# Kernel optimization log

Measured on AMD Instinct MI355X. Metric: run time of the kernel, lower is better.

## Reference

```python
import math
import jax, jax.numpy as jnp
import numpy as np

D_MODEL = 1024
NHEAD = 16
DK = D_MODEL // NHEAD
FACTOR = 5
B, L = 4, 8192
U = max(1, min(FACTOR * math.ceil(math.log(L + 1)), L))  # 50


def setup_inputs() -> dict:
    key = jax.random.key(0)
    ks = jax.random.split(key, 10)
    s = 1.0 / math.sqrt(D_MODEL)
    inp = {
        "x": jax.random.normal(ks[0], (B, L, D_MODEL), dtype=jnp.float32),
        "Wq": jax.random.normal(ks[1], (D_MODEL, D_MODEL), dtype=jnp.float32) * s,
        "bq": jnp.zeros((D_MODEL,), dtype=jnp.float32),
        "Wk": jax.random.normal(ks[2], (D_MODEL, D_MODEL), dtype=jnp.float32) * s,
        "bk": jnp.zeros((D_MODEL,), dtype=jnp.float32),
        "Wv": jax.random.normal(ks[3], (D_MODEL, D_MODEL), dtype=jnp.float32) * s,
        "bv": jnp.zeros((D_MODEL,), dtype=jnp.float32),
        "Wo": jax.random.normal(ks[4], (D_MODEL, D_MODEL), dtype=jnp.float32) * s,
        "bo": jnp.zeros((D_MODEL,), dtype=jnp.float32),
        # randperm(L)[:U] sample of key positions (constant, like torch.randperm)
        "idx_k": jax.random.permutation(ks[5], L)[:U].astype(jnp.int32),
    }
    return inp


def reference(x, Wq, bq, Wk, bk, Wv, bv, Wo, bo, idx_k):
    Bv, Lv, _ = x.shape
    H, dk = NHEAD, DK
    u = idx_k.shape[0]
    scale = 1.0 / math.sqrt(dk)

    # projections -> [B, H, L, dk]
    Q = (x @ Wq.T + bq).reshape(Bv, Lv, H, dk).transpose(0, 2, 1, 3)
    K = (x @ Wk.T + bk).reshape(Bv, Lv, H, dk).transpose(0, 2, 1, 3)
    V = (x @ Wv.T + bv).reshape(Bv, Lv, H, dk).transpose(0, 2, 1, 3)

    # sampled scores against u random keys: [B, H, L, u]
    K_samp = K[:, :, idx_k, :]
    scores = jnp.einsum("bhld,bhud->bhlu", Q, K_samp) * scale
    M = scores.max(-1) - scores.mean(-1)                 # [B, H, L]
    _, top_idx = jax.lax.top_k(M, u)                      # [B, H, u]

    # gather selected queries and attend against ALL keys
    Q_top = jnp.take_along_axis(Q, top_idx[..., None], axis=2)   # [B, H, u, dk]
    attn = jax.nn.softmax(jnp.einsum("bhud,bhld->bhul", Q_top, K) * scale, axis=-1)
    ctx_top = jnp.einsum("bhul,bhld->bhud", attn, V)              # [B, H, u, dk]

    # mean(V) fallback, scatter selected contexts back
    ctx = jnp.broadcast_to(V.mean(axis=2, keepdims=True), (Bv, H, Lv, dk))
    bidx = jnp.arange(Bv)[:, None, None]
    hidx = jnp.arange(H)[None, :, None]
    ctx = ctx.at[bidx, hidx, top_idx].set(ctx_top)

    ctx = ctx.transpose(0, 2, 1, 3).reshape(Bv, Lv, H * dk)
    return ctx @ Wo.T + bo
```

## Files before the change

kernel.cpp:

```cpp
#include <hip/hip_runtime.h>
#include <hip/hip_bf16.h>

#define B_ 4
#define L_ 8192
#define D_ 1024
#define H_ 16
#define SCALE 0.125f
#define NC 8
#define QPAD 64
#define RS 72

typedef __attribute__((ext_vector_type(8))) short bf16x8;
typedef __attribute__((ext_vector_type(4))) float f32x4;

__device__ __forceinline__ void gl2lds16(const void* g, void* s) {
    __builtin_amdgcn_global_load_lds(
        (const __attribute__((address_space(1))) unsigned int*)g,
        (__attribute__((address_space(3))) unsigned int*)s, 16, 0, 0);
}

__device__ __forceinline__ unsigned short bfbits(float a) {
    __hip_bfloat16 h = __float2bfloat16(a);
    return *(unsigned short*)&h;
}
__device__ __forceinline__ float bf2f(unsigned short u) {
    return __uint_as_float(((unsigned)u) << 16);
}

__global__ __launch_bounds__(256) void split3_kernel(const float* __restrict__ in,
        unsigned short* __restrict__ ph, unsigned short* __restrict__ pm,
        unsigned short* __restrict__ pl, int n4) {
    int i = blockIdx.x * 256 + threadIdx.x;
    if (i >= n4) return;
    float4 v = ((const float4*)in)[i];
    float c[4] = {v.x, v.y, v.z, v.w};
    unsigned short h[4], m[4], l[4];
    #pragma unroll
    for (int j = 0; j < 4; ++j) {
        float a = c[j];
        unsigned short hb = bfbits(a);
        float rh = a - bf2f(hb);
        unsigned short mb = bfbits(rh);
        float rm = rh - bf2f(mb);
        h[j] = hb; m[j] = mb; l[j] = bfbits(rm);
    }
    ((ushort4*)ph)[i] = *(ushort4*)h;
    ((ushort4*)pm)[i] = *(ushort4*)m;
    ((ushort4*)pl)[i] = *(ushort4*)l;
}

__global__ __launch_bounds__(256) void split2_kernel(const float* __restrict__ in,
        unsigned short* __restrict__ ph, unsigned short* __restrict__ pm, int n4) {
    int i = blockIdx.x * 256 + threadIdx.x;
    if (i >= n4) return;
    float4 v = ((const float4*)in)[i];
    float c[4] = {v.x, v.y, v.z, v.w};
    unsigned short h[4], m[4];
    #pragma unroll
    for (int j = 0; j < 4; ++j) {
        float a = c[j];
        unsigned short hb = bfbits(a);
        float rh = a - bf2f(hb);
        h[j] = hb; m[j] = bfbits(rh);
    }
    ((ushort4*)ph)[i] = *(ushort4*)h;
    ((ushort4*)pm)[i] = *(ushort4*)m;
}

__global__ __launch_bounds__(256) void xmean_kernel(const float* __restrict__ x,
                                                    float* __restrict__ xmean) {
    int c = blockIdx.x;
    int j = blockIdx.y * 256 + threadIdx.x;
    int b = blockIdx.z;
    const float* xp = x + ((size_t)b * L_ + (size_t)c * 256) * D_ + j;
    float s = 0.f;
    for (int l = 0; l < 256; ++l) s += xp[(size_t)l * D_];
    atomicAdd(&xmean[b * D_ + j], s * (1.0f / L_));
}

__global__ __launch_bounds__(256) void vecmat_kernel(const float* __restrict__ in,
                                                     const float* __restrict__ W,
                                                     const float* __restrict__ bias,
                                                     float* __restrict__ out) {
    __shared__ float vs[D_];
    int b = blockIdx.y;
    int j = blockIdx.x * 256 + threadIdx.x;
    for (int t = threadIdx.x; t < D_; t += 256) vs[t] = in[b * D_ + t];
    __syncthreads();
    const float* wr = W + (size_t)j * D_;
    float acc = 0.f;
    #pragma unroll 4
    for (int k = 0; k < D_; k += 4) {
        float4 w4 = *(const float4*)(wr + k);
        acc += vs[k] * w4.x + vs[k + 1] * w4.y + vs[k + 2] * w4.z + vs[k + 3] * w4.w;
    }
    out[b * D_ + j] = acc + bias[j];
}

__global__ __launch_bounds__(256) void ksamp_kernel(const float* __restrict__ x,
                                                    const float* __restrict__ Wk,
                                                    const float* __restrict__ bk,
                                                    const int* __restrict__ idx_k,
                                                    float* __restrict__ Ksamp, int U) {
    __shared__ float vs[D_];
    int u = blockIdx.x, b = blockIdx.y;
    int row = idx_k[u];
    const float* xp = x + ((size_t)b * L_ + row) * D_;
    for (int t = threadIdx.x; t < D_; t += 256) vs[t] = xp[t];
    __syncthreads();
    #pragma unroll
    for (int r = 0; r < 4; ++r) {
        int j = r * 256 + threadIdx.x;
        const float* wr = Wk + (size_t)j * D_;
        float acc = 0.f;
        #pragma unroll 4
        for (int k = 0; k < D_; k += 4) {
            float4 w4 = *(const float4*)(wr + k);
            acc += vs[k] * w4.x + vs[k + 1] * w4.y + vs[k + 2] * w4.z + vs[k + 3] * w4.w;
        }
        Ksamp[((size_t)b * U + u) * D_ + j] = acc + bk[j];
    }
}

#define TM 128
#define TN 128
#define BK 32
#define TSZ (TM * BK)

__global__ __launch_bounds__(256) void qkv_mfma(
    const unsigned short* __restrict__ xh, const unsigned short* __restrict__ xm,
    const unsigned short* __restrict__ xl,
    const unsigned short* __restrict__ qh, const unsigned short* __restrict__ qm,
    const unsigned short* __restrict__ ql,
    const unsigned short* __restrict__ kh, const unsigned short* __restrict__ km,
    const unsigned short* __restrict__ vh, const unsigned short* __restrict__ vm,
    const float* __restrict__ bq, const float* __restrict__ bk2, const float* __restrict__ bv,
    float* __restrict__ Q, __hip_bfloat16* __restrict__ Kb, __hip_bfloat16* __restrict__ Vb) {
    __shared__ __align__(16) unsigned short As[3][TSZ];
    __shared__ __align__(16) unsigned short Bs[3][TSZ];

    const int n0 = blockIdx.x * TN;
    const int m0 = blockIdx.y * TM;
    const int tid = threadIdx.x;

    const float* bias; int which; int nb;
    if (n0 < 1024)      { which = 0; nb = n0;        bias = bq;  }
    else if (n0 < 2048) { which = 1; nb = n0 - 1024; bias = bk2; }
    else                { which = 2; nb = n0 - 2048; bias = bv;  }

    const int srow = tid >> 2;
    const int scol = (tid & 3) * 8;

    const int wave = tid >> 6;
    const int lane = tid & 63;
    const int wm = (wave & 1) * 64;
    const int wn = (wave >> 1) * 64;
    const int fr = lane & 15;
    const int fk = (lane >> 4) * 8;
    const int rbase = (lane >> 4) * 4;

    f32x4 acc[4][4];
    #pragma unroll
    for (int i = 0; i < 4; ++i)
        #pragma unroll
        for (int j = 0; j < 4; ++j)
            acc[i][j] = (f32x4){0.f, 0.f, 0.f, 0.f};

    const size_t aBase = (size_t)(m0 + srow) * D_ + scol;
    const size_t bBase = (size_t)(nb + srow) * D_ + scol;

    bf16x8 af[4], bfv[4];
    auto loadA = [&](const unsigned short* t) {
        #pragma unroll
        for (int i = 0; i < 4; ++i)
            af[i] = *(const bf16x8*)(t + (wm + i * 16 + fr) * BK + fk);
    };
    auto loadB = [&](const unsigned short* t) {
        #pragma unroll
        for (int j = 0; j < 4; ++j)
            bfv[j] = *(const bf16x8*)(t + (wn + j * 16 + fr) * BK + fk);
    };
    auto prod = [&]() {
        #pragma unroll
        for (int i = 0; i < 4; ++i)
            #pragma unroll
            for (int j = 0; j < 4; ++j)
                acc[i][j] = __builtin_amdgcn_mfma_f32_16x16x32_bf16(
                    af[i], bfv[j], acc[i][j], 0, 0, 0);
    };
    auto stage = [&](const unsigned short* g, unsigned short* s, int kt, size_t base) {
        gl2lds16(g + base + kt, s + tid * 8);
        gl2lds16(g + base + (size_t)64 * D_ + kt, s + tid * 8 + 2048);
    };

    if (which == 0) {
        for (int kt = 0; kt < D_; kt += BK) {
            stage(xh, &As[0][0], kt, aBase);
            stage(xm, &As[1][0], kt, aBase);
            stage(xl, &As[2][0], kt, aBase);
            stage(qh, &Bs[0][0], kt, bBase);
            stage(qm, &Bs[1][0], kt, bBase);
            stage(ql, &Bs[2][0], kt, bBase);
            __syncthreads();
            loadA(&As[0][0]); loadB(&Bs[0][0]); prod();
            loadB(&Bs[1][0]); prod();
            loadB(&Bs[2][0]); prod();
            loadA(&As[1][0]); loadB(&Bs[0][0]); prod();
            loadB(&Bs[1][0]); prod();
            loadA(&As[2][0]); loadB(&Bs[0][0]); prod();
            __syncthreads();
        }
    } else {
        const unsigned short* Bh = (which == 1) ? kh : vh;
        const unsigned short* Bm = (which == 1) ? km : vm;
        for (int kt = 0; kt < D_; kt += BK) {
            stage(xh, &As[0][0], kt, aBase);
            stage(xm, &As[1][0], kt, aBase);
            stage(Bh, &Bs[0][0], kt, bBase);
            stage(Bm, &Bs[1][0], kt, bBase);
            __syncthreads();
            loadA(&As[0][0]); loadB(&Bs[0][0]); prod();
            loadB(&Bs[1][0]); prod();
            loadA(&As[1][0]); loadB(&Bs[0][0]); prod();
            __syncthreads();
        }
    }

    float biasv[4];
    #pragma unroll
    for (int j = 0; j < 4; ++j) biasv[j] = bias[nb + wn + j * 16 + fr];

    #pragma unroll
    for (int i = 0; i < 4; ++i) {
        #pragma unroll
        for (int r = 0; r < 4; ++r) {
            size_t row = (size_t)(m0 + wm + i * 16 + rbase + r);
            #pragma unroll
            for (int j = 0; j < 4; ++j) {
                float v = acc[i][j][r] + biasv[j];
                int n = nb + wn + j * 16 + fr;
                if (which == 0)      Q[row * D_ + n] = v;
                else if (which == 1) Kb[row * D_ + n] = __float2bfloat16(v);
                else                 Vb[row * D_ + n] = __float2bfloat16(v);
            }
        }
    }
}

__global__ __launch_bounds__(256) void m_kernel(const float* __restrict__ Q,
                                                const float* __restrict__ Ksamp,
                                                float* __restrict__ M, int U) {
    __shared__ float ks[64 * 64];
    int lc = blockIdx.x, h = blockIdx.y, b = blockIdx.z;
    for (int t = threadIdx.x; t < U * 64; t += 256) {
        int u = t >> 6, d = t & 63;
        ks[t] = Ksamp[((size_t)b * U + u) * D_ + h * 64 + d];
    }
    __syncthreads();
    int l = lc * 256 + threadIdx.x;
    const float* qp = Q + ((size_t)b * L_ + l) * D_ + h * 64;
    float q[64];
    #pragma unroll
    for (int i = 0; i < 16; ++i) *(float4*)&q[i * 4] = *(const float4*)(qp + i * 4);
    float mx = -INFINITY, sm = 0.f;
    for (int u = 0; u < U; ++u) {
        const float* kp = &ks[u * 64];
        float dot = 0.f;
        #pragma unroll
        for (int d = 0; d < 64; ++d) dot = fmaf(q[d], kp[d], dot);
        dot *= SCALE;
        mx = fmaxf(mx, dot);
        sm += dot;
    }
    M[((size_t)(b * H_ + h)) * L_ + l] = mx - sm / (float)U;
}

__global__ __launch_bounds__(256) void topk_kernel(const float* __restrict__ M,
                                                   int* __restrict__ topidx, int U) {
    __shared__ float vals[L_];
    __shared__ float wv[4];
    __shared__ int   wi[4];
    __shared__ int   sbest;
    int bh = blockIdx.x;
    const float* mp = M + (size_t)bh * L_;
    for (int t = threadIdx.x; t < L_; t += 256) vals[t] = mp[t];
    __syncthreads();

    float bv = -INFINITY; int bi = 0x7fffffff;
    for (int t = threadIdx.x; t < L_; t += 256) {
        float v = vals[t];
        if (v > bv || (v == bv && t < bi)) { bv = v; bi = t; }
    }
    const int lane = threadIdx.x & 63, wave = threadIdx.x >> 6;

    for (int u = 0; u < U; ++u) {
        float rv = bv; int ri = bi;
        #pragma unroll
        for (int s = 1; s < 64; s <<= 1) {
            float v2 = __shfl_xor(rv, s, 64);
            int   i2 = __shfl_xor(ri, s, 64);
            if (v2 > rv || (v2 == rv && i2 < ri)) { rv = v2; ri = i2; }
        }
        if (lane == 0) { wv[wave] = rv; wi[wave] = ri; }
        __syncthreads();
        if (threadIdx.x == 0) {
            float fv = wv[0]; int fi = wi[0];
            #pragma unroll
            for (int w = 1; w < 4; ++w) {
                if (wv[w] > fv || (wv[w] == fv && wi[w] < fi)) { fv = wv[w]; fi = wi[w]; }
            }
            topidx[bh * U + u] = fi;
            sbest = fi;
            vals[fi] = -INFINITY;
        }
        __syncthreads();
        int fi = sbest;
        if ((fi & 255) == threadIdx.x) {
            bv = -INFINITY; bi = 0x7fffffff;
            for (int t = threadIdx.x; t < L_; t += 256) {
                float v = vals[t];
                if (v > bv || (v == bv && t < bi)) { bv = v; bi = t; }
            }
        }
    }
}

__global__ __launch_bounds__(256) void attn_mfma(const float* __restrict__ Q,
        const __hip_bfloat16* __restrict__ Kb, const __hip_bfloat16* __restrict__ Vb,
        const int* __restrict__ topidx,
        float* __restrict__ part_m, float* __restrict__ part_s,
        float* __restrict__ part_acc, int U) {
    __shared__ __align__(16) unsigned short Qh[QPAD * RS];
    __shared__ __align__(16) unsigned short Qm[QPAD * RS];
    __shared__ __align__(16) unsigned short Ks[64 * RS];
    __shared__ __align__(16) unsigned short Vt[64 * RS];
    __shared__ __align__(16) unsigned short Ph[QPAD * RS];

    const int c = blockIdx.x, h = blockIdx.y, b = blockIdx.z;
    const int bh = b * H_ + h;
    const int tid = threadIdx.x;
    const int wave = tid >> 6, lane = tid & 63;
    const int w16 = wave * 16;
    const int fr = lane & 15;
    const int quad = lane >> 4;
    const int fk = quad * 8;
    const int l0 = c * (L_ / NC);

    {
        int u = tid >> 2;
        int d0 = (tid & 3) * 16;
        unsigned short hbuf[16], mbuf[16];
        if (u < U) {
            int row = topidx[bh * U + u];
            const float* qp = Q + ((size_t)b * L_ + row) * D_ + h * 64 + d0;
            #pragma unroll
            for (int i = 0; i < 16; ++i) {
                float v = qp[i] * SCALE;
                unsigned short hb = bfbits(v);
                hbuf[i] = hb;
                mbuf[i] = bfbits(v - bf2f(hb));
            }
        } else {
            #pragma unroll
            for (int i = 0; i < 16; ++i) { hbuf[i] = 0; mbuf[i] = 0; }
        }
        #pragma unroll
        for (int i = 0; i < 2; ++i) {
            *(uint4*)&Qh[u * RS + d0 + i * 8] = ((uint4*)hbuf)[i];
            *(uint4*)&Qm[u * RS + d0 + i * 8] = ((uint4*)mbuf)[i];
        }
    }

    const int kkey = tid >> 3, kd0 = (tid & 7) * 8;
    const int vkey = tid >> 2, vd0 = (tid & 3) * 16;
    const __hip_bfloat16* kbase = Kb + ((size_t)b * L_ + l0) * D_ + h * 64;
    const __hip_bfloat16* vbase = Vb + ((size_t)b * L_ + l0) * D_ + h * 64;

    uint4 kr0, kr1, vr0, vr1;
    auto loadKV = [&](int t) {
        const __hip_bfloat16* kp = kbase + (size_t)t * 64 * D_;
        const __hip_bfloat16* vp = vbase + (size_t)t * 64 * D_ + (size_t)vkey * D_ + vd0;
        kr0 = *(const uint4*)(kp + (size_t)kkey * D_ + kd0);
        kr1 = *(const uint4*)(kp + (size_t)(kkey + 32) * D_ + kd0);
        vr0 = *(const uint4*)(vp);
        vr1 = *(const uint4*)(vp + 8);
    };
    auto writeKV = [&]() {
        *(uint4*)&Ks[kkey * RS + kd0] = kr0;
        *(uint4*)&Ks[(kkey + 32) * RS + kd0] = kr1;
        unsigned short vb_[16];
        *(uint4*)&vb_[0] = vr0;
        *(uint4*)&vb_[8] = vr1;
        #pragma unroll
        for (int i = 0; i < 16; ++i) Vt[(vd0 + i) * RS + vkey] = vb_[i];
    };

    float m_r[4], s_r[4];
    f32x4 acc_o[4];
    #pragma unroll
    for (int r = 0; r < 4; ++r) { m_r[r] = -INFINITY; s_r[r] = 0.f; }
    #pragma unroll
    for (int n = 0; n < 4; ++n) acc_o[n] = (f32x4){0.f, 0.f, 0.f, 0.f};

    loadKV(0);
    writeKV();
    __syncthreads();

    const int NT = (L_ / NC) / 64;
    for (int t = 0; t < NT; ++t) {
        if (t + 1 < NT) loadKV(t + 1);

        f32x4 sacc[4];
        __builtin_amdgcn_s_setprio(1);
        #pragma unroll
        for (int n = 0; n < 4; ++n) {
            sacc[n] = (f32x4){0.f, 0.f, 0.f, 0.f};
            #pragma unroll
            for (int ks = 0; ks < 2; ++ks) {
                int k0 = ks * 32;
                bf16x8 ah = *(const bf16x8*)&Qh[(w16 + fr) * RS + k0 + fk];
                bf16x8 am = *(const bf16x8*)&Qm[(w16 + fr) * RS + k0 + fk];
                bf16x8 bb = *(const bf16x8*)&Ks[(n * 16 + fr) * RS + k0 + fk];
                sacc[n] = __builtin_amdgcn_mfma_f32_16x16x32_bf16(ah, bb, sacc[n], 0, 0, 0);
                sacc[n] = __builtin_amdgcn_mfma_f32_16x16x32_bf16(am, bb, sacc[n], 0, 0, 0);
            }
        }
        __builtin_amdgcn_s_setprio(0);

        float p[4][4];
        #pragma unroll
        for (int r = 0; r < 4; ++r) {
            float rowmax = fmaxf(fmaxf(sacc[0][r], sacc[1][r]),
                                 fmaxf(sacc[2][r], sacc[3][r]));
            #pragma unroll
            for (int msk = 1; msk <= 8; msk <<= 1)
                rowmax = fmaxf(rowmax, __shfl_xor(rowmax, msk, 64));
            float mnew = fmaxf(m_r[r], rowmax);
            float alpha = __expf(m_r[r] - mnew);
            float rowsum = 0.f;
            #pragma unroll
            for (int n = 0; n < 4; ++n) {
                p[n][r] = __expf(sacc[n][r] - mnew);
                rowsum += p[n][r];
            }
            #pragma unroll
            for (int msk = 1; msk <= 8; msk <<= 1)
                rowsum += __shfl_xor(rowsum, msk, 64);
            s_r[r] = s_r[r] * alpha + rowsum;
            m_r[r] = mnew;
            #pragma unroll
            for (int n = 0; n < 4; ++n) acc_o[n][r] *= alpha;
        }

        #pragma unroll
        for (int r = 0; r < 4; ++r)
            #pragma unroll
            for (int n = 0; n < 4; ++n)
                Ph[(w16 + quad * 4 + r) * RS + n * 16 + fr] = bfbits(p[n][r]);

        __builtin_amdgcn_s_setprio(1);
        #pragma unroll
        for (int n = 0; n < 4; ++n) {
            #pragma unroll
            for (int ks = 0; ks < 2; ++ks) {
                int k0 = ks * 32;
                bf16x8 pa = *(const bf16x8*)&Ph[(w16 + fr) * RS + k0 + fk];
                bf16x8 vb = *(const bf16x8*)&Vt[(n * 16 + fr) * RS + k0 + fk];
                acc_o[n] = __builtin_amdgcn_mfma_f32_16x16x32_bf16(pa, vb, acc_o[n], 0, 0, 0);
            }
        }
        __builtin_amdgcn_s_setprio(0);

        if (t + 1 < NT) {
            __syncthreads();
            writeKV();
            __syncthreads();
        }
    }

    #pragma unroll
    for (int r = 0; r < 4; ++r) {
        int q = w16 + quad * 4 + r;
        if (q < U) {
            size_t base = ((size_t)(bh * QPAD + q)) * NC + c;
            if (fr == 0) { part_m[base] = m_r[r]; part_s[base] = s_r[r]; }
            #pragma unroll
            for (int n = 0; n < 4; ++n)
                part_acc[base * 64 + n * 16 + fr] = acc_o[n][r];
        }
    }
}

__global__ __launch_bounds__(64) void attn_combine(const float* __restrict__ part_m,
        const float* __restrict__ part_s, const float* __restrict__ part_acc,
        float* __restrict__ ctx_top, int U) {
    int u = blockIdx.x, h = blockIdx.y, b = blockIdx.z;
    int bh = b * H_ + h;
    int d = threadIdx.x;
    size_t base = ((size_t)(bh * QPAD + u)) * NC;
    float M = -INFINITY;
    #pragma unroll
    for (int c = 0; c < NC; ++c) M = fmaxf(M, part_m[base + c]);
    float S = 0.f, A = 0.f;
    #pragma unroll
    for (int c = 0; c < NC; ++c) {
        float f = __expf(part_m[base + c] - M);
        S += part_s[base + c] * f;
        A += part_acc[(base + c) * 64 + d] * f;
    }
    ctx_top[(((size_t)bh) * U + u) * 64 + d] = A / S;
}

__global__ __launch_bounds__(256) void fill_base_kernel(const float* __restrict__ base,
                                                        float* __restrict__ out) {
    size_t i = (size_t)blockIdx.x * 256 + threadIdx.x;
    int col4 = (int)(i & 255);
    int b = (int)(i >> 21);
    ((float4*)out)[i] = ((const float4*)base)[b * 256 + col4];
}

__global__ __launch_bounds__(256) void delta_kernel(const float* __restrict__ ctx_top,
        const float* __restrict__ vmean, const float* __restrict__ Wo,
        const int* __restrict__ topidx, float* __restrict__ out, int U) {
    __shared__ float cd[64];
    int u = blockIdx.x, h = blockIdx.y, b = blockIdx.z;
    int row = topidx[(b * H_ + h) * U + u];
    if (threadIdx.x < 64) {
        cd[threadIdx.x] = ctx_top[(((size_t)(b * H_ + h)) * U + u) * 64 + threadIdx.x]
                        - vmean[b * D_ + h * 64 + threadIdx.x];
    }
    __syncthreads();
    float* op = out + ((size_t)b * L_ + row) * D_;
    #pragma unroll
    for (int r = 0; r < 4; ++r) {
        int j = r * 256 + threadIdx.x;
        const float* wr = Wo + (size_t)j * D_ + h * 64;
        float dlt = 0.f;
        #pragma unroll
        for (int k = 0; k < 64; k += 4) {
            float4 w4 = *(const float4*)(wr + k);
            dlt += cd[k] * w4.x + cd[k + 1] * w4.y + cd[k + 2] * w4.z + cd[k + 3] * w4.w;
        }
        atomicAdd(op + j, dlt);
    }
}

extern "C" void kernel_launch(void* const* d_in, const int* in_sizes, int n_in,
                              void* d_out, int out_size, void* d_ws, size_t ws_size,
                              hipStream_t stream) {
    const float* x   = (const float*)d_in[0];
    const float* Wq  = (const float*)d_in[1];
    const float* bq  = (const float*)d_in[2];
    const float* Wk  = (const float*)d_in[3];
    const float* bk  = (const float*)d_in[4];
    const float* Wv  = (const float*)d_in[5];
    const float* bv  = (const float*)d_in[6];
    const float* Wo  = (const float*)d_in[7];
    const float* bo  = (const float*)d_in[8];
    const int* idx_k = (const int*)d_in[9];
    const int U = in_sizes[9];
    float* out = (float*)d_out;
    (void)n_in; (void)ws_size;

    char* ws = (char*)d_ws;
    size_t off = 0;
    auto alloc = [&](size_t bytes) -> void* {
        void* p = ws + off;
        off += (bytes + 255) & ~(size_t)255;
        return p;
    };
    float* Q              = (float*)alloc((size_t)B_ * L_ * D_ * 4);
    __hip_bfloat16* Kb    = (__hip_bfloat16*)alloc((size_t)B_ * L_ * D_ * 2);
    __hip_bfloat16* Vb    = (__hip_bfloat16*)alloc((size_t)B_ * L_ * D_ * 2);
    unsigned short* xh    = (unsigned short*)alloc((size_t)B_ * L_ * D_ * 2);
    unsigned short* xm    = (unsigned short*)alloc((size_t)B_ * L_ * D_ * 2);
    unsigned short* xl    = (unsigned short*)alloc((size_t)B_ * L_ * D_ * 2);
    unsigned short* wqh   = (unsigned short*)alloc((size_t)D_ * D_ * 2);
    unsigned short* wqm   = (unsigned short*)alloc((size_t)D_ * D_ * 2);
    unsigned short* wql   = (unsigned short*)alloc((size_t)D_ * D_ * 2);
    unsigned short* wkh   = (unsigned short*)alloc((size_t)D_ * D_ * 2);
    unsigned short* wkm   = (unsigned short*)alloc((size_t)D_ * D_ * 2);
    unsigned short* wvh   = (unsigned short*)alloc((size_t)D_ * D_ * 2);
    unsigned short* wvm   = (unsigned short*)alloc((size_t)D_ * D_ * 2);
    float* Ksamp          = (float*)alloc((size_t)B_ * 64 * D_ * 4);
    float* Mbuf           = (float*)alloc((size_t)B_ * H_ * L_ * 4);
    int*   topidx         = (int*)alloc((size_t)B_ * H_ * 64 * 4);
    float* xmean          = (float*)alloc((size_t)B_ * D_ * 4);
    float* vmean          = (float*)alloc((size_t)B_ * D_ * 4);
    float* base           = (float*)alloc((size_t)B_ * D_ * 4);
    float* ctxt           = (float*)alloc((size_t)B_ * H_ * 64 * 64 * 4);
    float* part_m         = (float*)alloc((size_t)B_ * H_ * QPAD * NC * 4);
    float* part_s         = (float*)alloc((size_t)B_ * H_ * QPAD * NC * 4);
    float* part_acc       = (float*)alloc((size_t)B_ * H_ * QPAD * NC * 64 * 4);

    hipMemsetAsync(xmean, 0, (size_t)B_ * D_ * 4, stream);
    xmean_kernel<<<dim3(32, 4, B_), 256, 0, stream>>>(x, xmean);
    vecmat_kernel<<<dim3(4, B_), 256, 0, stream>>>(xmean, Wv, bv, vmean);
    vecmat_kernel<<<dim3(4, B_), 256, 0, stream>>>(vmean, Wo, bo, base);
    ksamp_kernel<<<dim3(U, B_), 256, 0, stream>>>(x, Wk, bk, idx_k, Ksamp, U);

    const int n4x = B_ * L_ * D_ / 4;
    const int n4w = D_ * D_ / 4;
    split3_kernel<<<dim3(n4x / 256), 256, 0, stream>>>(x, xh, xm, xl, n4x);
    split3_kernel<<<dim3(n4w / 256), 256, 0, stream>>>(Wq, wqh, wqm, wql, n4w);
    split2_kernel<<<dim3(n4w / 256), 256, 0, stream>>>(Wk, wkh, wkm, n4w);
    split2_kernel<<<dim3(n4w / 256), 256, 0, stream>>>(Wv, wvh, wvm, n4w);

    qkv_mfma<<<dim3(24, 256), 256, 0, stream>>>(xh, xm, xl, wqh, wqm, wql,
                                                wkh, wkm, wvh, wvm,
                                                bq, bk, bv, Q, Kb, Vb);

    m_kernel<<<dim3(32, H_, B_), 256, 0, stream>>>(Q, Ksamp, Mbuf, U);
    topk_kernel<<<dim3(B_ * H_), 256, 0, stream>>>(Mbuf, topidx, U);
    attn_mfma<<<dim3(NC, H_, B_), 256, 0, stream>>>(Q, Kb, Vb, topidx,
                                                    part_m, part_s, part_acc, U);
    attn_combine<<<dim3(U, H_, B_), 64, 0, stream>>>(part_m, part_s, part_acc, ctxt, U);
    fill_base_kernel<<<dim3(out_size / 4 / 256), 256, 0, stream>>>(base, out);
    delta_kernel<<<dim3(U, H_, B_), 256, 0, stream>>>(ctxt, vmean, Wo, topidx, out, U);
}
```

Before: 1.770 ms.

## Replace iterative argmax top-k with radix-select and double attention chunk count

The top-k kernel, which ran U serial argmax rounds each with block-wide reductions and barriers, is replaced by a 4-pass 8-bit radix select over order-preserving integer keys. Elements strictly above the threshold key are emitted through an atomic counter, and ties are resolved by index rank. Output order now differs from sorted top-k order, which only matters if later stages rely on that order. Separately, NC goes from 8 to 16, doubling the key-chunk split in attention for more parallelism at the cost of more partial results to merge.

```diff
diff --git a/kernel.cpp b/kernel.cpp
--- a/kernel.cpp
+++ b/kernel.cpp
@@ -6,7 +6,7 @@
 #define D_ 1024
 #define H_ 16
 #define SCALE 0.125f
-#define NC 8
+#define NC 16
 #define QPAD 64
 #define RS 72
 
@@ -277,51 +277,67 @@
 
 __global__ __launch_bounds__(256) void topk_kernel(const float* __restrict__ M,
                                                    int* __restrict__ topidx, int U) {
-    __shared__ float vals[L_];
-    __shared__ float wv[4];
-    __shared__ int   wi[4];
-    __shared__ int   sbest;
-    int bh = blockIdx.x;
+    __shared__ unsigned keys[L_];
+    __shared__ int      eqlist[L_];
+    __shared__ int      hist[256];
+    __shared__ unsigned sprefix;
+    __shared__ int      sneed, cgt, ceq;
+
+    const int bh = blockIdx.x;
+    const int tid = threadIdx.x;
     const float* mp = M + (size_t)bh * L_;
-    for (int t = threadIdx.x; t < L_; t += 256) vals[t] = mp[t];
+
+    for (int t = tid; t < L_; t += 256) {
+        unsigned s = __float_as_uint(mp[t]);
+        keys[t] = (s & 0x80000000u) ? ~s : (s | 0x80000000u);
+    }
+    if (tid == 0) { cgt = 0; ceq = 0; }
     __syncthreads();
 
-    float bv = -INFINITY; int bi = 0x7fffffff;
-    for (int t = threadIdx.x; t < L_; t += 256) {
-        float v = vals[t];
-        if (v > bv || (v == bv && t < bi)) { bv = v; bi = t; }
-    }
-    const int lane = threadIdx.x & 63, wave = threadIdx.x >> 6;
-
-    for (int u = 0; u < U; ++u) {
-        float rv = bv; int ri = bi;
-        #pragma unroll
-        for (int s = 1; s < 64; s <<= 1) {
-            float v2 = __shfl_xor(rv, s, 64);
-            int   i2 = __shfl_xor(ri, s, 64);
-            if (v2 > rv || (v2 == rv && i2 < ri)) { rv = v2; ri = i2; }
-        }
-        if (lane == 0) { wv[wave] = rv; wi[wave] = ri; }
+    unsigned prefix = 0;
+    int need = U;
+    for (int shift = 24; shift >= 0; shift -= 8) {
+        hist[tid] = 0;
         __syncthreads();
-        if (threadIdx.x == 0) {
-            float fv = wv[0]; int fi = wi[0];
-            #pragma unroll
-            for (int w = 1; w < 4; ++w) {
-                if (wv[w] > fv || (wv[w] == fv && wi[w] < fi)) { fv = wv[w]; fi = wi[w]; }
+        for (int t = tid; t < L_; t += 256) {
+            unsigned k = keys[t];
+            bool ok = (shift == 24) ||
+                      ((k >> (shift + 8)) == (prefix >> (shift + 8)));
+            if (ok) atomicAdd(&hist[(k >> shift) & 255], 1);
+        }
+        __syncthreads();
+        if (tid == 0) {
+            int acc = 0, b = 255;
+            for (; b > 0; --b) {
+                if (acc + hist[b] >= need) break;
+                acc += hist[b];
             }
-            topidx[bh * U + u] = fi;
-            sbest = fi;
-            vals[fi] = -INFINITY;
+            sneed = need - acc;
+            sprefix = prefix | ((unsigned)b << shift);
         }
         __syncthreads();
-        int fi = sbest;
-        if ((fi & 255) == threadIdx.x) {
-            bv = -INFINITY; bi = 0x7fffffff;
-            for (int t = threadIdx.x; t < L_; t += 256) {
-                float v = vals[t];
-                if (v > bv || (v == bv && t < bi)) { bv = v; bi = t; }
-            }
-        }
+        prefix = sprefix;
+        need = sneed;
+        __syncthreads();
+    }
+    const unsigned vkey = prefix;
+
+    for (int t = tid; t < L_; t += 256) {
+        unsigned k = keys[t];
+        if (k > vkey) {
+            int pos = atomicAdd(&cgt, 1);
+            topidx[bh * U + pos] = t;
+        } else if (k == vkey) {
+            int p = atomicAdd(&ceq, 1);
+            eqlist[p] = t;
+        }
+    }
+    __syncthreads();
+    const int s = ceq, r = need, base = U - r;
+    for (int i = tid; i < s; i += 256) {
+        int mine = eqlist[i], rank = 0;
+        for (int j = 0; j < s; ++j) rank += (eqlist[j] < mine);
+        if (rank < r) topidx[bh * U + base + rank] = mine;
     }
 }
 
```

New measurement: 1.611 ms. 9.0% less time.
